# Performance work log

Measured on AMD Instinct MI355X. Metric: run time of the kernel, lower is better.

The kernel has to match this reference:

```python
import jax, jax.numpy as jnp
import numpy as np

B, T, LEADS = 16, 3600, 12
P = 9; S = T // P          # 400 patches
DP = 128                   # d_patch / codebook dim
DM = 256                   # d_model
H = 8; HD = DM // H        # heads, head_dim
NL = 6                     # transformer layers
V = 512                    # codebook size
RH = 64                    # residual CNN hidden
BETA = 0.25


def conv1d(x, w, b, pad, stride=1):
    # x: (B,C,T), w: (O,I,K) pytorch layout
    y = jax.lax.conv_general_dilated(x, w, (stride,), [(pad, pad)],
                                     dimension_numbers=('NCH', 'OIH', 'NCH'))
    return y + b[None, :, None]


def layer_norm(x, g, b, eps=1e-5):
    m = jnp.mean(x, -1, keepdims=True)
    v = jnp.mean(jnp.square(x - m), -1, keepdims=True)
    return (x - m) * jax.lax.rsqrt(v + eps) * g + b


def gelu(x):
    return jax.nn.gelu(x, approximate=False)  # matches torch nn.GELU default


def setup_inputs() -> dict:
    key = jax.random.key(0)
    ks = iter(jax.random.split(key, 64))
    def rn(shape, s=0.02):
        return (s * jax.random.normal(next(ks), shape)).astype(jnp.float32)
    inp = {}
    inp['x'] = jax.random.normal(next(ks), (B, T, LEADS), dtype=jnp.float32)
    # PatchEncoder
    inp['pe_w1'] = rn((DP // 2, LEADS, 3)); inp['pe_b1'] = rn((DP // 2,))
    inp['pe_w2'] = rn((DP, DP // 2, 3));    inp['pe_b2'] = rn((DP,))
    inp['pe_pw'] = rn((DP, DP, P));         inp['pe_pb'] = rn((DP,))
    inp['pe_g'] = jnp.ones((DP,), jnp.float32); inp['pe_bb'] = jnp.zeros((DP,), jnp.float32)
    # VQ codebook (uniform +-1/V as in torch init)
    inp['cb'] = jax.random.uniform(next(ks), (V, DP), jnp.float32, -1.0 / V, 1.0 / V)
    # token_proj
    inp['tp_w'] = rn((DM, DP)); inp['tp_b'] = rn((DM,))
    inp['tp_g'] = jnp.ones((DM,), jnp.float32); inp['tp_bb'] = jnp.zeros((DM,), jnp.float32)
    # transformer layers (stacked over NL)
    inp['ln1_g'] = jnp.ones((NL, DM), jnp.float32); inp['ln1_b'] = jnp.zeros((NL, DM), jnp.float32)
    inp['inw'] = rn((NL, 3 * DM, DM));  inp['inb'] = rn((NL, 3 * DM))
    inp['ow'] = rn((NL, DM, DM));       inp['ob'] = rn((NL, DM))
    inp['ln2_g'] = jnp.ones((NL, DM), jnp.float32); inp['ln2_b'] = jnp.zeros((NL, DM), jnp.float32)
    inp['f1w'] = rn((NL, 4 * DM, DM));  inp['f1b'] = rn((NL, 4 * DM))
    inp['f2w'] = rn((NL, DM, 4 * DM));  inp['f2b'] = rn((NL, DM))
    inp['slopes'] = (1.0 + 0.1 * jax.random.normal(next(ks), (NL, H))).astype(jnp.float32)
    # final norm
    inp['fn_g'] = jnp.ones((DM,), jnp.float32); inp['fn_b'] = jnp.zeros((DM,), jnp.float32)
    # PatchDecoder: ConvTranspose1d weight (in=DM, out=DM//2, k=P)
    inp['up_w'] = rn((DM, DM // 2, P)); inp['up_b'] = rn((DM // 2,))
    inp['d1w'] = rn((DM // 4, DM // 2, 5)); inp['d1b'] = rn((DM // 4,))
    inp['d2w'] = rn((LEADS, DM // 4, 3));   inp['d2b'] = rn((LEADS,))
    # ResidualCNN
    inp['r1w'] = rn((RH, LEADS, 7)); inp['r1b'] = rn((RH,))
    inp['r2w'] = rn((RH, RH, 5));    inp['r2b'] = rn((RH,))
    inp['r3w'] = rn((RH, RH, 3));    inp['r3b'] = rn((RH,))
    inp['r4w'] = rn((LEADS, RH, 1)); inp['r4b'] = rn((LEADS,))
    inp['alpha'] = jnp.float32(0.5)
    return inp


def _forward(x, pe_w1, pe_b1, pe_w2, pe_b2, pe_pw, pe_pb, pe_g, pe_bb, cb,
             tp_w, tp_b, tp_g, tp_bb, ln1_g, ln1_b, inw, inb, ow, ob,
             ln2_g, ln2_b, f1w, f1b, f2w, f2b, slopes, fn_g, fn_b,
             up_w, up_b, d1w, d1b, d2w, d2b,
             r1w, r1b, r2w, r2b, r3w, r3b, r4w, r4b, alpha):
    Bs = x.shape[0]
    sg = jax.lax.stop_gradient
    # --- PatchEncoder: (B,T,L) -> (B,S,DP) ---
    h = x.transpose(0, 2, 1)                      # (B,L,T)
    h = gelu(conv1d(h, pe_w1, pe_b1, 1))
    h = gelu(conv1d(h, pe_w2, pe_b2, 1))
    h = conv1d(h, pe_pw, pe_pb, 0, stride=P)      # (B,DP,S)
    z_e = layer_norm(h.transpose(0, 2, 1), pe_g, pe_bb)   # (B,S,DP)
    # --- VQ codebook with STE ---
    zf = z_e.reshape(-1, DP)
    dist = (jnp.sum(zf * zf, 1, keepdims=True) + jnp.sum(cb * cb, 1)[None, :]
            - 2.0 * zf @ cb.T)                    # (B*S, V)
    tokens = jnp.argmin(dist, axis=1)
    zq = cb[tokens]                               # (B*S, DP)
    commit = jnp.mean(jnp.square(sg(zq) - zf)) + BETA * jnp.mean(jnp.square(zq - sg(zf)))
    zq_ste = (zf + sg(zq - zf)).reshape(Bs, S, DP)
    # --- token projection ---
    h = layer_norm(zq_ste @ tp_w.T + tp_b, tp_g, tp_bb)   # (B,S,DM)
    # --- transformer with relative-position bias ---
    pos = jnp.arange(S)
    rel = jnp.abs(pos[:, None] - pos[None, :]).astype(h.dtype)  # (S,S)
    scale = 1.0 / jnp.sqrt(jnp.float32(HD))
    for l in range(NL):
        bias = -jnp.abs(slopes[l])[:, None, None] * rel[None]   # (H,S,S)
        xn = layer_norm(h, ln1_g[l], ln1_b[l])
        qkv = xn @ inw[l].T + inb[l]
        q, k, v = jnp.split(qkv, 3, axis=-1)
        q = q.reshape(Bs, S, H, HD); k = k.reshape(Bs, S, H, HD); v = v.reshape(Bs, S, H, HD)
        logits = jnp.einsum('bqhd,bkhd->bhqk', q, k) * scale + bias[None]
        attn = jax.nn.softmax(logits, axis=-1)
        o = jnp.einsum('bhqk,bkhd->bqhd', attn, v).reshape(Bs, S, DM)
        h = h + o @ ow[l].T + ob[l]
        hn = layer_norm(h, ln2_g[l], ln2_b[l])
        h = h + gelu(hn @ f1w[l].T + f1b[l]) @ f2w[l].T + f2b[l]
    h = layer_norm(h, fn_g, fn_b)
    # --- PatchDecoder: (B,S,DM) -> (B,T,L) ---
    hc = h.transpose(0, 2, 1)                     # (B,DM,S)
    # ConvTranspose1d with stride==kernel==P, no overlap -> pure einsum
    u = jnp.einsum('bds,dok->bosk', hc, up_w).reshape(Bs, DM // 2, S * P) + up_b[None, :, None]
    u = gelu(u)
    u = gelu(conv1d(u, d1w, d1b, 2))
    u = conv1d(u, d2w, d2b, 1)                    # (B,L,T)
    decoded = u.transpose(0, 2, 1)
    # --- ResidualCNN on raw input ---
    r = x.transpose(0, 2, 1)
    r = gelu(conv1d(r, r1w, r1b, 3))
    r = gelu(conv1d(r, r2w, r2b, 2))
    r = gelu(conv1d(r, r3w, r3b, 1))
    r = conv1d(r, r4w, r4b, 0)
    residual = r.transpose(0, 2, 1)
    out = decoded + alpha * residual
    return out, commit


def reference(x, pe_w1, pe_b1, pe_w2, pe_b2, pe_pw, pe_pb, pe_g, pe_bb, cb,
              tp_w, tp_b, tp_g, tp_bb, ln1_g, ln1_b, inw, inb, ow, ob,
              ln2_g, ln2_b, f1w, f1b, f2w, f2b, slopes, fn_g, fn_b,
              up_w, up_b, d1w, d1b, d2w, d2b,
              r1w, r1b, r2w, r2b, r3w, r3b, r4w, r4b, alpha):
    return _forward(x, pe_w1, pe_b1, pe_w2, pe_b2, pe_pw, pe_pb, pe_g, pe_bb, cb,
                    tp_w, tp_b, tp_g, tp_bb, ln1_g, ln1_b, inw, inb, ow, ob,
                    ln2_g, ln2_b, f1w, f1b, f2w, f2b, slopes, fn_g, fn_b,
                    up_w, up_b, d1w, d1b, d2w, d2b,
                    r1w, r1b, r2w, r2b, r3w, r3b, r4w, r4b, alpha)
```

## Files before the change

### kernel.cpp

```cpp
#include <hip/hip_runtime.h>
#include <hip/hip_bf16.h>
#include <math.h>

#define BATCH 16
#define TLEN 3600
#define LEADS 12
#define PP 9
#define SS 400
#define DP 128
#define DM 256
#define NH 8
#define HD 32
#define NLAY 6
#define VV 512
#define RH 64

typedef __attribute__((ext_vector_type(8))) short short8b;
typedef __attribute__((ext_vector_type(4))) float f32x4;

__device__ __forceinline__ float gelu_f(float x) {
    return 0.5f * x * (1.0f + erff(x * 0.70710678118654752f));
}

__device__ __forceinline__ unsigned short f2bf(float f) {
// ... 352 lines not shown
                #pragma unroll
                for (int e = 0; e < 8; ++e) {
                    unsigned short h = f2bf(vv[e]);
                    h8[e] = (short)h;
                    l8[e] = (short)f2bf(vv[e] - bf2f(h));
                }
                *(short8b*)&Ah[srow][sc + g * 8] = h8;
                *(short8b*)&Al[srow][sc + g * 8] = l8;
            }
            const unsigned short* gh = ch + (size_t)(c0 + srow) * DP + k0 + sc;
            const unsigned short* gl = cl + (size_t)(c0 + srow) * DP + k0 + sc;
            *(short8b*)&Bh[srow][sc] = *(const short8b*)gh;
            *(short8b*)&Bh[srow][sc + 8] = *(const short8b*)(gh + 8);
            *(short8b*)&Bl[srow][sc] = *(const short8b*)gl;
            *(short8b*)&Bl[srow][sc + 8] = *(const short8b*)(gl + 8);
        }
        __syncthreads();
        short8b afh[4], afl[4], bfh[4], bfl[4];
        #pragma unroll
        for (int i = 0; i < 4; ++i) {
            afh[i] = *(const short8b*)&Ah[wr0 + i * 16 + fr][kg];
            afl[i] = *(const short8b*)&Al[wr0 + i * 16 + fr][kg];
            bfh[i] = *(const short8b*)&Bh[wc0 + i * 16 + fr][kg];
            bfl[i] = *(const short8b*)&Bl[wc0 + i * 16 + fr][kg];
        }
        #pragma unroll
        for (int i = 0; i < 4; ++i)
            #pragma unroll
            for (int j = 0; j < 4; ++j) {
                acc[i][j] = __builtin_amdgcn_mfma_f32_16x16x32_bf16(afh[i], bfh[j], acc[i][j], 0, 0, 0);
                acc[i][j] = __builtin_amdgcn_mfma_f32_16x16x32_bf16(afh[i], bfl[j], acc[i][j], 0, 0, 0);
                acc[i][j] = __builtin_amdgcn_mfma_f32_16x16x32_bf16(afl[i], bfh[j], acc[i][j], 0, 0, 0);
            }
    }
    const int orow = (lane >> 4) * 4, ocol = lane & 15;
    #pragma unroll
    for (int i = 0; i < 4; ++i)
        #pragma unroll
        for (int r = 0; r < 4; ++r) {
            int row = wr0 + i * 16 + orow + r;
            float bv = 1e30f; int bi = 0;
            #pragma unroll
            for (int j = 0; j < 4; ++j) {
                int col = c0 + wc0 + j * 16 + ocol;
                float d = cbn[col] - 2.0f * acc[i][j][r];
                if (d < bv || (d == bv && col < bi)) { bv = d; bi = col; }
            }
            #pragma unroll
            for (int o = 1; o < 16; o <<= 1) {
                float ov = __shfl_xor(bv, o);
                int oi = __shfl_xor(bi, o);
                if (ov < bv || (ov == bv && oi < bi)) { bv = ov; bi = oi; }
            }
            if (ocol == 0) { bwv[row][w & 1] = bv; bwi[row][w & 1] = bi; }
        }
    __syncthreads();
    if (tid < 128) {
        float v0 = bwv[tid][0], v1 = bwv[tid][1];
        int i0 = bwi[tid][0], i1 = bwi[tid][1];
        bool sel = (v1 < v0) || (v1 == v0 && i1 < i0);
        pval[(size_t)blockIdx.x * M + gm0 + tid] = sel ? v1 : v0;
        pidx[(size_t)blockIdx.x * M + gm0 + tid] = sel ? i1 : i0;
    }
}

__global__ __launch_bounds__(128) void vqfin_k(const float* __restrict__ ze,
                                               const float* __restrict__ cb,
                                               const float* __restrict__ pval,
                                               const int* __restrict__ pidx,
                                               unsigned short* __restrict__ zqb,
                                               float* __restrict__ vqs,
                                               int M) {
    const int row = blockIdx.x, tid = threadIdx.x;
    __shared__ float sm[2];
    __shared__ int tok_s;
    if (tid == 0) {
        float bv = pval[row]; int bi = pidx[row];
        #pragma unroll
        for (int z = 1; z < 4; ++z) {
            float v = pval[(size_t)z * M + row]; int ix = pidx[(size_t)z * M + row];
            if (v < bv || (v == bv && ix < bi)) { bv = v; bi = ix; }
        }
        tok_s = bi;
    }
    __syncthreads();
    int tok = tok_s;
    float qv = cb[(size_t)tok * DP + tid];
    float zv = ze[(size_t)row * DP + tid];
    zqb[(size_t)row * DP + tid] = f2bf(qv);
    float d = qv - zv;
    float tot = block_sum_128(d * d, sm);
    if (tid == 0) vqs[row] = tot;
}

template <int CI, int K, int PAD>
__global__ __launch_bounds__(256) void mfconv_k(const unsigned short* __restrict__ in,
                                                const unsigned short* __restrict__ wpk,
                                                const float* __restrict__ bias,
                                                unsigned short* __restrict__ out) {
    constexpr int CIC = (CI > 64) ? 64 : CI;
    constexpr int NCH = CI / CIC;
    constexpr int TROWS = 128 + K - 1;
    constexpr int CQ = CIC / 8;
    __shared__ __align__(16) unsigned short in_s[TROWS][CIC + 8];
    __shared__ __align__(16) unsigned short w_s[K][64][CIC + 8];
    const int b = blockIdx.z;
    const int t0 = blockIdx.x * 128;
    const int tid = threadIdx.x;
    const int w = tid >> 6, lane = tid & 63;
    const int fr = lane & 15, kg = (lane >> 4) * 8;
    f32x4 acc[2][4];
    #pragma unroll
    for (int i = 0; i < 2; ++i)
        #pragma unroll
        for (int j = 0; j < 4; ++j) acc[i][j] = (f32x4){0.f, 0.f, 0.f, 0.f};
    for (int ch = 0; ch < NCH; ++ch) {
        const int c0 = ch * CIC;
        if (ch) __syncthreads();
        for (int u = tid; u < TROWS * CQ; u += 256) {
            int row = u / CQ, q = u - row * CQ;
            int t = t0 + row - PAD;
            short8b v = (short8b){0, 0, 0, 0, 0, 0, 0, 0};
            if (t >= 0 && t < TLEN)
                v = *(const short8b*)&in[((size_t)(b * TLEN + t)) * CI + c0 + q * 8];
            *(short8b*)&in_s[row][q * 8] = v;
        }
        for (int u = tid; u < K * 64 * CQ; u += 256) {
            int q = u % CQ; int rest = u / CQ; int co = rest & 63; int k = rest >> 6;
            *(short8b*)&w_s[k][co][q * 8] =
                *(const short8b*)&wpk[((size_t)(k * 64 + co)) * CI + c0 + q * 8];
        }
        __syncthreads();
        #pragma unroll
        for (int k = 0; k < K; ++k) {
            #pragma unroll
            for (int c32 = 0; c32 < CIC / 32; ++c32) {
                short8b a0 = *(const short8b*)&in_s[w * 32 + fr + k][c32 * 32 + kg];
                short8b a1 = *(const short8b*)&in_s[w * 32 + 16 + fr + k][c32 * 32 + kg];
                short8b b0 = *(const short8b*)&w_s[k][fr][c32 * 32 + kg];
                short8b b1 = *(const short8b*)&w_s[k][16 + fr][c32 * 32 + kg];
                short8b b2 = *(const short8b*)&w_s[k][32 + fr][c32 * 32 + kg];
                short8b b3 = *(const short8b*)&w_s[k][48 + fr][c32 * 32 + kg];
                acc[0][0] = __builtin_amdgcn_mfma_f32_16x16x32_bf16(a0, b0, acc[0][0], 0, 0, 0);
                acc[0][1] = __builtin_amdgcn_mfma_f32_16x16x32_bf16(a0, b1, acc[0][1], 0, 0, 0);
                acc[0][2] = __builtin_amdgcn_mfma_f32_16x16x32_bf16(a0, b2, acc[0][2], 0, 0, 0);
                acc[0][3] = __builtin_amdgcn_mfma_f32_16x16x32_bf16(a0, b3, acc[0][3], 0, 0, 0);
                acc[1][0] = __builtin_amdgcn_mfma_f32_16x16x32_bf16(a1, b0, acc[1][0], 0, 0, 0);
                acc[1][1] = __builtin_amdgcn_mfma_f32_16x16x32_bf16(a1, b1, acc[1][1], 0, 0, 0);
                acc[1][2] = __builtin_amdgcn_mfma_f32_16x16x32_bf16(a1, b2, acc[1][2], 0, 0, 0);
                acc[1][3] = __builtin_amdgcn_mfma_f32_16x16x32_bf16(a1, b3, acc[1][3], 0, 0, 0);
            }
        }
    }
    const int orow = (lane >> 4) * 4, ocol = lane & 15;
    #pragma unroll
    for (int i = 0; i < 2; ++i)
        #pragma unroll
        for (int j = 0; j < 4; ++j) {
            const int co = j * 16 + ocol;
            const float bv = bias[co];
            #pragma unroll
            for (int r = 0; r < 4; ++r) {
                int t = t0 + w * 32 + i * 16 + orow + r;
                if (t < TLEN)
                    out[((size_t)(b * TLEN + t)) * 64 + co] = f2bf(gelu_f(acc[i][j][r] + bv));
            }
        }
}

template <int ACT, int RES, int OUTBF>
__global__ __launch_bounds__(256) void bgemm_k(const unsigned short* __restrict__ A,
                                               const unsigned short* __restrict__ W,
                                               const float* __restrict__ bias,
                                               const float* __restrict__ res,
                                               void* __restrict__ Cv,
                                               int M, int N, int K) {
    __shared__ __align__(16) unsigned short As[128][40];
    __shared__ __align__(16) unsigned short Bs[128][40];
    const int tid = threadIdx.x;
    const int gm0 = blockIdx.y * 128, gn0 = blockIdx.x * 128;
    const int w = tid >> 6, lane = tid & 63;
    const int wr0 = (w >> 1) * 64, wc0 = (w & 1) * 64;
    const int srow = tid >> 1, sc = (tid & 1) * 16;
    const unsigned short* ga = A + (size_t)(gm0 + srow) * K + sc;
    const unsigned short* gb = W + (size_t)(gn0 + srow) * K + sc;
    short8b ra0 = *(const short8b*)(ga), ra1 = *(const short8b*)(ga + 8);
    short8b rb0 = *(const short8b*)(gb), rb1 = *(const short8b*)(gb + 8);
    f32x4 acc[4][4];
    #pragma unroll
    for (int i = 0; i < 4; ++i)
        #pragma unroll
        for (int j = 0; j < 4; ++j) acc[i][j] = (f32x4){0.f, 0.f, 0.f, 0.f};
    const int fr = lane & 15, kg = (lane >> 4) * 8;
    const int nstep = K >> 5;
    for (int s = 0; s < nstep; ++s) {
        __syncthreads();
        *(short8b*)&As[srow][sc] = ra0; *(short8b*)&As[srow][sc + 8] = ra1;
        *(short8b*)&Bs[srow][sc] = rb0; *(short8b*)&Bs[srow][sc + 8] = rb1;
        __syncthreads();
        if (s + 1 < nstep) {
            ga += 32; gb += 32;
            ra0 = *(const short8b*)(ga); ra1 = *(const short8b*)(ga + 8);
            rb0 = *(const short8b*)(gb); rb1 = *(const short8b*)(gb + 8);
        }
        short8b af[4], bf[4];
        #pragma unroll
        for (int i = 0; i < 4; ++i) {
            af[i] = *(const short8b*)&As[wr0 + i * 16 + fr][kg];
            bf[i] = *(const short8b*)&Bs[wc0 + i * 16 + fr][kg];
        }
        #pragma unroll
        for (int i = 0; i < 4; ++i)
            #pragma unroll
            for (int j = 0; j < 4; ++j)
                acc[i][j] = __builtin_amdgcn_mfma_f32_16x16x32_bf16(af[i], bf[j], acc[i][j], 0, 0, 0);
    }
    const int orow = (lane >> 4) * 4, ocol = lane & 15;
    #pragma unroll
    for (int i = 0; i < 4; ++i) {
        #pragma unroll
        for (int j = 0; j < 4; ++j) {
            const int colg = gn0 + wc0 + j * 16 + ocol;
            const float bsv = bias[colg];
            #pragma unroll
            for (int r = 0; r < 4; ++r) {
                const int rowg = gm0 + wr0 + i * 16 + orow + r;
                float v = acc[i][j][r] + bsv;
                if (ACT) v = gelu_f(v);
                if (RES) v += res[(size_t)rowg * N + colg];
                if (OUTBF) ((unsigned short*)Cv)[(size_t)rowg * N + colg] = f2bf(v);
                else ((float*)Cv)[(size_t)rowg * N + colg] = v;
            }
        }
    }
}

template <int ACT, int RES, int OUTBF>
__global__ __launch_bounds__(256) void bgemm64_k(const unsigned short* __restrict__ A,
                                                 const unsigned short* __restrict__ W,
                                                 const float* __restrict__ bias,
                                                 const float* __restrict__ res,
                                                 void* __restrict__ Cv,
                                                 int M, int N, int K) {
    __shared__ __align__(16) unsigned short As[64][40];
    __shared__ __align__(16) unsigned short Bs[128][40];
    const int tid = threadIdx.x;
    const int gm0 = blockIdx.y * 64, gn0 = blockIdx.x * 128;
    const int w = tid >> 6, lane = tid & 63;
    const int wc0 = w * 32;
    const int arow = tid >> 2, ac = (tid & 3) * 8;
    const int brow = tid >> 1, bc = (tid & 1) * 16;
    const unsigned short* ga = A + (size_t)(gm0 + arow) * K + ac;
    const unsigned short* gb = W + (size_t)(gn0 + brow) * K + bc;
    short8b ra0 = *(const short8b*)(ga);
    short8b rb0 = *(const short8b*)(gb), rb1 = *(const short8b*)(gb + 8);
    f32x4 acc[4][2];
    #pragma unroll
    for (int i = 0; i < 4; ++i)
        #pragma unroll
        for (int j = 0; j < 2; ++j) acc[i][j] = (f32x4){0.f, 0.f, 0.f, 0.f};
    const int fr = lane & 15, kg = (lane >> 4) * 8;
    const int nstep = K >> 5;
    for (int s = 0; s < nstep; ++s) {
        __syncthreads();
        *(short8b*)&As[arow][ac] = ra0;
        *(short8b*)&Bs[brow][bc] = rb0; *(short8b*)&Bs[brow][bc + 8] = rb1;
        __syncthreads();
        if (s + 1 < nstep) {
            ga += 32; gb += 32;
            ra0 = *(const short8b*)(ga);
            rb0 = *(const short8b*)(gb); rb1 = *(const short8b*)(gb + 8);
        }
        short8b af[4], bf[2];
        #pragma unroll
        for (int i = 0; i < 4; ++i) af[i] = *(const short8b*)&As[i * 16 + fr][kg];
        #pragma unroll
        for (int j = 0; j < 2; ++j) bf[j] = *(const short8b*)&Bs[wc0 + j * 16 + fr][kg];
        #pragma unroll
        for (int i = 0; i < 4; ++i)
            #pragma unroll
            for (int j = 0; j < 2; ++j)
                acc[i][j] = __builtin_amdgcn_mfma_f32_16x16x32_bf16(af[i], bf[j], acc[i][j], 0, 0, 0);
    }
    const int orow = (lane >> 4) * 4, ocol = lane & 15;
    #pragma unroll
    for (int i = 0; i < 4; ++i) {
        #pragma unroll
        for (int j = 0; j < 2; ++j) {
            const int colg = gn0 + wc0 + j * 16 + ocol;
            const float bsv = bias[colg];
            #pragma unroll
            for (int r = 0; r < 4; ++r) {
                const int rowg = gm0 + i * 16 + orow + r;
                float v = acc[i][j][r] + bsv;
                if (ACT) v = gelu_f(v);
                if (RES) v += res[(size_t)rowg * N + colg];
                if (OUTBF) ((unsigned short*)Cv)[(size_t)rowg * N + colg] = f2bf(v);
                else ((float*)Cv)[(size_t)rowg * N + colg] = v;
            }
        }
    }
}

__global__ void tobf_k(const float* __restrict__ in, unsigned short* __restrict__ out, int n) {
    int i = blockIdx.x * 256 + threadIdx.x;
    if (i < n) out[i] = f2bf(in[i]);
}

__global__ void cpack_k(const float* __restrict__ w, unsigned short* __restrict__ out,
                        int Co, int CI, int K) {
    int idx = blockIdx.x * 256 + threadIdx.x;
    if (idx < Co * CI * K) {
        int ci = idx % CI; int rest = idx / CI; int co = rest % Co; int k = rest / Co;
        out[idx] = f2bf(w[((size_t)co * CI + ci) * K + k]);
    }
}

__global__ void upwt2_k(const float* __restrict__ w, const float* __restrict__ bsrc,
                        unsigned short* __restrict__ out, float* __restrict__ b2) {
    int idx = blockIdx.x * 256 + threadIdx.x;
    if (idx < 1152 * 256) {
        int d = idx & 255, n = idx >> 8;
        int o = n & 127, k = n >> 7;
        out[(size_t)n * 256 + d] = f2bf(w[(size_t)d * 1152 + o * 9 + k]);
    }
    if (idx < 1152) b2[idx] = bsrc[idx & 127];
}

__global__ __launch_bounds__(128) void ln128s_k(const float* __restrict__ part,
                                                const float* __restrict__ bias,
                                                const float* __restrict__ g,
                                                const float* __restrict__ bb,
                                                float* __restrict__ out,
                                                int M) {
    int row = blockIdx.x, tid = threadIdx.x;
    __shared__ float sm[2];
    size_t stride = (size_t)M * DP;
    size_t base = (size_t)row * DP + tid;
    float v = bias[tid];
    #pragma unroll
    for (int s2 = 0; s2 < 6; ++s2) v += part[base + (size_t)s2 * stride];
    float mean = block_sum_128(v, sm) * (1.0f / DP);
    float d = v - mean;
    float var = block_sum_128(d * d, sm) * (1.0f / DP);
    out[(size_t)row * DP + tid] = d * rsqrtf(var + 1e-5f) * g[tid] + bb[tid];
}

__global__ void cbnorm_k(const float* __restrict__ cb, float* __restrict__ cbn) {
    int c = blockIdx.x * 256 + threadIdx.x;
    if (c < VV) {
        const float* cr = cb + (size_t)c * DP;
        float s = 0;
        for (int i = 0; i < DP; ++i) s += cr[i] * cr[i];
        cbn[c] = s;
    }
}

__global__ void vqreduce_k(const float* __restrict__ vqs, float* __restrict__ out) {
    float s = 0;
    for (int i = threadIdx.x; i < BATCH * SS; i += 256) s += vqs[i];
    __shared__ float sm[4];
    s = block_sum_256(s, sm);
    if (threadIdx.x == 0) out[0] = s * (1.25f / (float)(BATCH * SS * DP));
}

template <int OUTBF>
__global__ __launch_bounds__(256) void lnw_k(const float* __restrict__ in,
                                             const float* __restrict__ g,
                                             const float* __restrict__ bb,
                                             void* __restrict__ out) {
    const int row = blockIdx.x * 4 + (threadIdx.x >> 6);
    const int lane = threadIdx.x & 63;
    float4 v = *(const float4*)&in[(size_t)row * DM + lane * 4];
    float s = v.x + v.y + v.z + v.w;
    #pragma unroll
    for (int o = 1; o < 64; o <<= 1) s += __shfl_xor(s, o);
    float mean = s * (1.0f / DM);
    float dx = v.x - mean, dy = v.y - mean, dz = v.z - mean, dw = v.w - mean;
    float vv = dx * dx + dy * dy + dz * dz + dw * dw;
    #pragma unroll
    for (int o = 1; o < 64; o <<= 1) vv += __shfl_xor(vv, o);
    float rstd = rsqrtf(vv * (1.0f / DM) + 1e-5f);
    float4 gv = *(const float4*)&g[lane * 4];
    float4 bv = *(const float4*)&bb[lane * 4];
    float o0 = dx * rstd * gv.x + bv.x;
    float o1 = dy * rstd * gv.y + bv.y;
    float o2 = dz * rstd * gv.z + bv.z;
    float o3 = dw * rstd * gv.w + bv.w;
    if (OUTBF) {
        unsigned long long pk = (unsigned long long)f2bf(o0)
                              | ((unsigned long long)f2bf(o1) << 16)
                              | ((unsigned long long)f2bf(o2) << 32)
                              | ((unsigned long long)f2bf(o3) << 48);
        *(unsigned long long*)((unsigned short*)out + (size_t)row * DM + lane * 4) = pk;
    } else {
        float4 o4; o4.x = o0; o4.y = o1; o4.z = o2; o4.w = o3;
        *(float4*)((float*)out + (size_t)row * DM + lane * 4) = o4;
    }
}

__global__ __launch_bounds__(256) void fattn2_k(const unsigned short* __restrict__ qkv,
                                                const float* __restrict__ slopes,
                                                unsigned short* __restrict__ out) {
    __shared__ __align__(16) unsigned short Qs[128][40];
    __shared__ __align__(16) unsigned short Ks[64][40];
    __shared__ __align__(16) unsigned short Vt[32][72];
    __shared__ __align__(16) unsigned short Ps[4][32][72];
    const int qb = blockIdx.x, hh = blockIdx.y, b = blockIdx.z;
    const int tid = threadIdx.x;
    const int w = tid >> 6, lane = tid & 63;
    const int lr = lane & 15, lg = lane >> 4;
    const float slope = fabsf(slopes[hh]);
    const unsigned short* base = qkv + (size_t)b * SS * (3 * DM);
    {
        int row = tid >> 1, c = (tid & 1) * 16;
        int q = qb * 128 + row; q = q < SS ? q : SS - 1;
        const unsigned short* src = base + (size_t)q * (3 * DM) + hh * HD + c;
        *(short8b*)&Qs[row][c] = *(const short8b*)src;
        *(short8b*)&Qs[row][c + 8] = *(const short8b*)(src + 8);
    }
    __syncthreads();
    short8b qa[2];
    qa[0] = *(const short8b*)&Qs[w * 32 + lr][lg * 8];
    qa[1] = *(const short8b*)&Qs[w * 32 + 16 + lr][lg * 8];
    float m_run[2][4], l_run[2][4];
    #pragma unroll
    for (int f = 0; f < 2; ++f)
        #pragma unroll
        for (int r = 0; r < 4; ++r) { m_run[f][r] = -1e30f; l_run[f][r] = 0.f; }
    f32x4 of0[2], of1[2];
    of0[0] = of0[1] = of1[0] = of1[1] = (f32x4){0.f, 0.f, 0.f, 0.f};
    const int qg0[2] = { qb * 128 + w * 32 + lg * 4, qb * 128 + w * 32 + 16 + lg * 4 };
    for (int kt = 0; kt < SS; kt += 64) {
        const int tl = (SS - kt) < 64 ? (SS - kt) : 64;
        const int nks = tl >> 4;
        __syncthreads();
        {
            int row = tid >> 2, c = (tid & 3) * 8;
            if (row < tl) {
                *(short8b*)&Ks[row][c] =
                    *(const short8b*)(base + (size_t)(kt + row) * (3 * DM) + DM + hh * HD + c);
                short8b v8 = *(const short8b*)(base + (size_t)(kt + row) * (3 * DM) + 2 * DM + hh * HD + c);
                #pragma unroll
                for (int j = 0; j < 8; ++j) Vt[c + j][row] = ((unsigned short*)&v8)[j];
            }
        }
        __syncthreads();
        f32x4 sf[2][4];
        #pragma unroll
        for (int ks = 0; ks < 4; ++ks) {
            if (ks < nks) {
                short8b kb8 = *(const short8b*)&Ks[ks * 16 + lr][lg * 8];
                sf[0][ks] = __builtin_amdgcn_mfma_f32_16x16x32_bf16(qa[0], kb8, (f32x4){0.f, 0.f, 0.f, 0.f}, 0, 0, 0);
                sf[1][ks] = __builtin_amdgcn_mfma_f32_16x16x32_bf16(qa[1], kb8, (f32x4){0.f, 0.f, 0.f, 0.f}, 0, 0, 0);
            }
        }
        #pragma unroll
        for (int f = 0; f < 2; ++f) {
            float pv[4][4];
            #pragma unroll
            for (int r = 0; r < 4; ++r) {
                float tmax = -1e30f;
                #pragma unroll
                for (int ks = 0; ks < 4; ++ks) {
                    if (ks < nks) {
                        float sv = sf[f][ks][r] * 0.17677669529663687f
                                 - slope * fabsf((float)(qg0[f] + r - (kt + ks * 16 + lr)));
                        pv[ks][r] = sv;
                        tmax = fmaxf(tmax, sv);
                    }
                }
                #pragma unroll
                for (int o = 1; o < 16; o <<= 1) tmax = fmaxf(tmax, __shfl_xor(tmax, o));
                float mnew = fmaxf(m_run[f][r], tmax);
                float sc = __expf(m_run[f][r] - mnew);
                m_run[f][r] = mnew;
                float tsum = 0.f;
                #pragma unroll
                for (int ks = 0; ks < 4; ++ks) {
                    if (ks < nks) {
                        float e = __expf(pv[ks][r] - mnew);
                        pv[ks][r] = e;
                        tsum += e;
                    }
                }
                #pragma unroll
                for (int o = 1; o < 16; o <<= 1) tsum += __shfl_xor(tsum, o);
                l_run[f][r] = l_run[f][r] * sc + tsum;
                of0[f][r] *= sc; of1[f][r] *= sc;
            }
            #pragma unroll
            for (int ks = 0; ks < 4; ++ks)
                #pragma unroll
                for (int r = 0; r < 4; ++r)
                    Ps[w][f * 16 + lg * 4 + r][ks * 16 + lr] = (ks < nks) ? f2bf(pv[ks][r]) : (unsigned short)0;
        }
        #pragma unroll
        for (int kc = 0; kc < 64; kc += 32) {
            if (kc < nks * 16) {
                short8b vb0 = *(const short8b*)&Vt[lr][kc + lg * 8];
                short8b vb1 = *(const short8b*)&Vt[16 + lr][kc + lg * 8];
                #pragma unroll
                for (int f = 0; f < 2; ++f) {
                    short8b pa = *(const short8b*)&Ps[w][f * 16 + lr][kc + lg * 8];
                    of0[f] = __builtin_amdgcn_mfma_f32_16x16x32_bf16(pa, vb0, of0[f], 0, 0, 0);
                    of1[f] = __builtin_amdgcn_mfma_f32_16x16x32_bf16(pa, vb1, of1[f], 0, 0, 0);
                }
            }
        }
    }
    #pragma unroll
    for (int f = 0; f < 2; ++f)
        #pragma unroll
        for (int r = 0; r < 4; ++r) {
            int q = qg0[f] + r;
            if (q < SS) {
                float inv = 1.0f / l_run[f][r];
                out[((size_t)(b * SS + q)) * DM + hh * HD + lr] = f2bf(of0[f][r] * inv);
                out[((size_t)(b * SS + q)) * DM + hh * HD + 16 + lr] = f2bf(of1[f][r] * inv);
            }
        }
}

__global__ __launch_bounds__(256) void final2_k(const unsigned short* __restrict__ ud1,
                                                const unsigned short* __restrict__ r3i,
                                                const float* __restrict__ d2w,
                                                const float* __restrict__ d2b,
                                                const float* __restrict__ r4w,
                                                const float* __restrict__ r4b,
                                                const float* __restrict__ alpha,
                                                float* __restrict__ out) {
    __shared__ float u_s[64][66];
    __shared__ float r_s[64][64];
    __shared__ float wd_s[64][3][12];
    __shared__ float wr_s[64][12];
    __shared__ float o_s[64][12];
    const int b = blockIdx.z, t0 = blockIdx.x * 64, tid = threadIdx.x;
    for (int u2 = tid; u2 < 66 * 8; u2 += 256) {
        int j = u2 >> 3, q = u2 & 7;
        int t = t0 + j - 1;
        short8b v = (short8b){0, 0, 0, 0, 0, 0, 0, 0};
        if (t >= 0 && t < TLEN) v = *(const short8b*)&ud1[((size_t)(b * TLEN + t)) * 64 + q * 8];
        #pragma unroll
        for (int i = 0; i < 8; ++i) u_s[q * 8 + i][j] = bf2f((unsigned short)v[i]);
    }
    for (int u2 = tid; u2 < 64 * 8; u2 += 256) {
        int j = u2 >> 3, q = u2 & 7;
        int t = t0 + j;
        short8b v = (short8b){0, 0, 0, 0, 0, 0, 0, 0};
        if (t < TLEN) v = *(const short8b*)&r3i[((size_t)(b * TLEN + t)) * 64 + q * 8];
        #pragma unroll
        for (int i = 0; i < 8; ++i) r_s[q * 8 + i][j] = bf2f((unsigned short)v[i]);
    }
    for (int idx = tid; idx < 64 * 3 * 12; idx += 256) {
        int l = idx % 12, k = (idx / 12) % 3, ci = idx / 36;
        wd_s[ci][k][l] = d2w[(l * 64 + ci) * 3 + k];
    }
    for (int idx = tid; idx < 64 * 12; idx += 256) {
        int l = idx % 12, ci = idx / 12;
        wr_s[ci][l] = r4w[l * 64 + ci];
    }
    __syncthreads();
    const int tl = tid & 63, lg = tid >> 6;
    float accD[3] = {}, accR[3] = {};
    for (int ci = 0; ci < 64; ++ci) {
        float a0 = u_s[ci][tl], a1 = u_s[ci][tl + 1], a2 = u_s[ci][tl + 2];
        float rv = r_s[ci][tl];
        #pragma unroll
        for (int c = 0; c < 3; ++c) {
            int l = lg * 3 + c;
            accD[c] += a0 * wd_s[ci][0][l] + a1 * wd_s[ci][1][l] + a2 * wd_s[ci][2][l];
            accR[c] = fmaf(rv, wr_s[ci][l], accR[c]);
        }
    }
    float al = alpha[0];
    #pragma unroll
    for (int c = 0; c < 3; ++c) {
        int l = lg * 3 + c;
        o_s[tl][l] = accD[c] + d2b[l] + al * (accR[c] + r4b[l]);
    }
    __syncthreads();
    for (int idx = tid; idx < 64 * 12; idx += 256) {
        int t = t0 + idx / 12;
        if (t < TLEN) out[((size_t)b * TLEN + t) * 12 + idx % 12] = o_s[idx / 12][idx % 12];
    }
}

extern "C" void kernel_launch(void* const* d_in, const int* in_sizes, int n_in,
                              void* d_out, int out_size, void* d_ws, size_t ws_size,
                              hipStream_t stream) {
    const float* x     = (const float*)d_in[0];
    const float* pe_w1 = (const float*)d_in[1];
    const float* pe_b1 = (const float*)d_in[2];
    const float* pe_w2 = (const float*)d_in[3];
    const float* pe_b2 = (const float*)d_in[4];
    const float* pe_pw = (const float*)d_in[5];
    const float* pe_pb = (const float*)d_in[6];
    const float* pe_g  = (const float*)d_in[7];
    const float* pe_bb = (const float*)d_in[8];
    const float* cb    = (const float*)d_in[9];
    const float* tp_w  = (const float*)d_in[10];
    const float* tp_b  = (const float*)d_in[11];
    const float* tp_g  = (const float*)d_in[12];
    const float* tp_bb = (const float*)d_in[13];
    const float* ln1_g = (const float*)d_in[14];
    const float* ln1_b = (const float*)d_in[15];
    const float* inw   = (const float*)d_in[16];
    const float* inb   = (const float*)d_in[17];
    const float* ow    = (const float*)d_in[18];
    const float* ob    = (const float*)d_in[19];
    const float* ln2_g = (const float*)d_in[20];
    const float* ln2_b = (const float*)d_in[21];
    const float* f1w   = (const float*)d_in[22];
    const float* f1b   = (const float*)d_in[23];
    const float* f2w   = (const float*)d_in[24];
    const float* f2b   = (const float*)d_in[25];
    const float* slopes= (const float*)d_in[26];
    const float* fn_g  = (const float*)d_in[27];
    const float* fn_b  = (const float*)d_in[28];
    const float* up_w  = (const float*)d_in[29];
    const float* up_b  = (const float*)d_in[30];
    const float* d1w   = (const float*)d_in[31];
    const float* d1b   = (const float*)d_in[32];
    const float* d2w   = (const float*)d_in[33];
    const float* d2b   = (const float*)d_in[34];
    const float* r1w   = (const float*)d_in[35];
    const float* r1b   = (const float*)d_in[36];
    const float* r2w   = (const float*)d_in[37];
    const float* r2b   = (const float*)d_in[38];
    const float* r3w   = (const float*)d_in[39];
    const float* r3b   = (const float*)d_in[40];
    const float* r4w   = (const float*)d_in[41];
    const float* r4b   = (const float*)d_in[42];
    const float* alpha = (const float*)d_in[43];

    float* W = (float*)d_ws;
    size_t off = 0;
    auto alloc = [&](size_t n) { float* p = W + off; off += (n + 3) & ~(size_t)3; return p; };
    const size_t M = (size_t)BATCH * SS;
    float* A    = alloc((size_t)BATCH * DP * TLEN);
    float* Bb   = alloc((size_t)BATCH * 64 * TLEN);
    float* ze   = alloc(M * DP);
    float* tx   = alloc(M * DM);
    float* hb   = alloc(M * DM);
    float* qf   = alloc(M * 3 * DM);
    float* cbn  = alloc(VV);
    float* vqs  = alloc(M);
    float* upb2 = alloc(1152);
    float* pval = alloc(4 * M);
    int*   pidx = (int*)alloc(4 * M);
    unsigned short* zqb  = (unsigned short*)alloc(M * DP / 2);
    unsigned short* xnb  = (unsigned short*)alloc(M * DM / 2);
    unsigned short* aob  = (unsigned short*)alloc(M * DM / 2);
    float* pgpart        = qf;
    unsigned short* qkvb = (unsigned short*)qf;
    unsigned short* ffb  = (unsigned short*)qf;
    unsigned short* utm  = (unsigned short*)qf;
    unsigned short* inwb = (unsigned short*)alloc((size_t)NLAY * 3 * DM * DM / 2);
    unsigned short* owb  = (unsigned short*)alloc((size_t)NLAY * DM * DM / 2);
    unsigned short* f1wb = (unsigned short*)alloc((size_t)NLAY * 4 * DM * DM / 2);
    unsigned short* f2wb = (unsigned short*)alloc((size_t)NLAY * 4 * DM * DM / 2);
    unsigned short* tpwb = (unsigned short*)alloc((size_t)DM * DP / 2);
    unsigned short* upwb = (unsigned short*)alloc((size_t)1152 * DM / 2);
    unsigned short* pwh  = (unsigned short*)alloc((size_t)128 * 1152 / 2);
    unsigned short* pwl  = (unsigned short*)alloc((size_t)128 * 1152 / 2);
    unsigned short* w2h  = (unsigned short*)alloc((size_t)3 * 128 * 64 / 2);
    unsigned short* w2l  = (unsigned short*)alloc((size_t)3 * 128 * 64 / 2);
    unsigned short* cbh  = (unsigned short*)alloc((size_t)VV * DP / 2);
    unsigned short* cbl  = (unsigned short*)alloc((size_t)VV * DP / 2);
    unsigned short* r2pk = (unsigned short*)alloc((size_t)64 * 64 * 5 / 2);
    unsigned short* r3pk = (unsigned short*)alloc((size_t)64 * 64 * 3 / 2 + 2);
    unsigned short* d1pk = (unsigned short*)alloc((size_t)64 * 128 * 5 / 2);
    unsigned short* r1tm = (unsigned short*)alloc((size_t)BATCH * TLEN * 64 / 2);
    unsigned short* r2tm = (unsigned short*)alloc((size_t)BATCH * TLEN * 64 / 2);
    unsigned short* r3tm = (unsigned short*)alloc((size_t)BATCH * TLEN * 64 / 2);
    unsigned short* d1tm = (unsigned short*)alloc((size_t)BATCH * TLEN * 64 / 2);
    if (off * sizeof(float) > ws_size) return;

    float* outp = (float*)d_out;
    const dim3 cgrid(57, 1, BATCH);
    const dim3 mgrid(29, 1, BATCH);

    tobf_k<<<(NLAY * 3 * DM * DM + 255) / 256, 256, 0, stream>>>(inw, inwb, NLAY * 3 * DM * DM);
    tobf_k<<<(NLAY * DM * DM + 255) / 256, 256, 0, stream>>>(ow, owb, NLAY * DM * DM);
    tobf_k<<<(NLAY * 4 * DM * DM + 255) / 256, 256, 0, stream>>>(f1w, f1wb, NLAY * 4 * DM * DM);
    tobf_k<<<(NLAY * 4 * DM * DM + 255) / 256, 256, 0, stream>>>(f2w, f2wb, NLAY * 4 * DM * DM);
    tobf_k<<<(DM * DP + 255) / 256, 256, 0, stream>>>(tp_w, tpwb, DM * DP);
    upwt2_k<<<(1152 * 256 + 255) / 256, 256, 0, stream>>>(up_w, up_b, upwb, upb2);
    pwpack3_k<<<(128 * 1152 + 255) / 256, 256, 0, stream>>>(pe_pw, pwh, pwl);
    pwpack2_k<<<(3 * 128 * 64 + 255) / 256, 256, 0, stream>>>(pe_w2, w2h, w2l);
    cbpack_k<<<(VV * DP + 255) / 256, 256, 0, stream>>>(cb, cbh, cbl);
    cpack_k<<<(64 * 64 * 5 + 255) / 256, 256, 0, stream>>>(r2w, r2pk, 64, 64, 5);
    cpack_k<<<(64 * 64 * 3 + 255) / 256, 256, 0, stream>>>(r3w, r3pk, 64, 64, 3);
    cpack_k<<<(64 * 128 * 5 + 255) / 256, 256, 0, stream>>>(d1w, d1pk, 64, 128, 5);

    enc1_k<<<dim3(57, BATCH), 256, 0, stream>>>(x, pe_w1, pe_b1, r1w, r1b, Bb, r1tm);

    pe2m_k<<<dim3(29, BATCH), 256, 0, stream>>>(Bb, w2h, w2l, pe_b2, A);
    cbnorm_k<<<2, 256, 0, stream>>>(cb, cbn);
    pproj3_k<<<dim3(1, M / 128, 6), 256, 0, stream>>>(A, pwh, pwl, pgpart, M);
    ln128s_k<<<M, 128, 0, stream>>>(pgpart, pe_pb, pe_g, pe_bb, ze, M);
    vq3_k<<<dim3(4, M / 128), 256, 0, stream>>>(ze, cbh, cbl, cbn, pval, pidx, M);
    vqfin_k<<<M, 128, 0, stream>>>(ze, cb, pval, pidx, zqb, vqs, M);
    vqreduce_k<<<1, 256, 0, stream>>>(vqs, outp + (size_t)BATCH * TLEN * LEADS);

    mfconv_k<64, 5, 2><<<mgrid, 256, 0, stream>>>(r1tm, r2pk, r2b, r2tm);
    mfconv_k<64, 3, 1><<<mgrid, 256, 0, stream>>>(r2tm, r3pk, r3b, r3tm);

    bgemm64_k<0, 0, 0><<<dim3(DM / 128, M / 64), 256, 0, stream>>>(zqb, tpwb, tp_b, nullptr, tx, M, DM, DP);
    lnw_k<0><<<M / 4, 256, 0, stream>>>(tx, tp_g, tp_bb, hb);

    for (int l = 0; l < NLAY; ++l) {
        lnw_k<1><<<M / 4, 256, 0, stream>>>(hb, ln1_g + l * DM, ln1_b + l * DM, xnb);
        bgemm_k<0, 0, 1><<<dim3(3 * DM / 128, M / 128), 256, 0, stream>>>(
            xnb, inwb + (size_t)l * 3 * DM * DM, inb + l * 3 * DM, nullptr, qkvb, M, 3 * DM, DM);
        fattn2_k<<<dim3((SS + 127) / 128, NH, BATCH), 256, 0, stream>>>(qkvb, slopes + l * NH, aob);
        bgemm64_k<0, 1, 0><<<dim3(DM / 128, M / 64), 256, 0, stream>>>(
            aob, owb + (size_t)l * DM * DM, ob + l * DM, hb, hb, M, DM, DM);
        lnw_k<1><<<M / 4, 256, 0, stream>>>(hb, ln2_g + l * DM, ln2_b + l * DM, xnb);
        bgemm_k<1, 0, 1><<<dim3(4 * DM / 128, M / 128), 256, 0, stream>>>(
            xnb, f1wb + (size_t)l * 4 * DM * DM, f1b + l * 4 * DM, nullptr, ffb, M, 4 * DM, DM);
        bgemm64_k<0, 1, 0><<<dim3(DM / 128, M / 64), 256, 0, stream>>>(
            ffb, f2wb + (size_t)l * 4 * DM * DM, f2b + l * DM, hb, hb, M, DM, 4 * DM);
    }
    lnw_k<1><<<M / 4, 256, 0, stream>>>(hb, fn_g, fn_b, xnb);

    bgemm_k<1, 0, 1><<<dim3(1152 / 128, M / 128), 256, 0, stream>>>(xnb, upwb, upb2, nullptr, utm, M, 1152, DM);
    mfconv_k<128, 5, 2><<<mgrid, 256, 0, stream>>>(utm, d1pk, d1b, d1tm);

    final2_k<<<cgrid, 256, 0, stream>>>(d1tm, r3tm, d2w, d2b, r4w, r4b, alpha, outp);
}
```

Measured before the change: 790.2 us.

## Fuse residual GEMMs with following LayerNorm and shrink attention query tile

Adds a GEMM kernel that computes a full 256-wide output row block (32 rows per block), adds bias and residual, writes the fp32 hidden state, then applies the next LayerNorm in-kernel and writes the bf16 normalized input. This replaces the separate out-proj/FFN2 GEMMs and the LN launches inside the layer loop, removing launches and a reread of the hidden state. Attention is changed to 64-query tiles (one 16-row fragment per wave), doubling the grid for better occupancy at the cost of reloading K/V more often. The fused GEMM uses a small 32-row tile and unpipelined register prefetch, which may lower MFMA efficiency.

```diff
diff --git a/kernel.cpp b/kernel.cpp
--- a/kernel.cpp
+++ b/kernel.cpp
@@ -678,6 +678,99 @@
     }
 }
 
+__global__ __launch_bounds__(256) void bgemmln_k(const unsigned short* __restrict__ A,
+                                                 const unsigned short* __restrict__ W,
+                                                 const float* __restrict__ bias,
+                                                 const float* __restrict__ res,
+                                                 float* __restrict__ hbout,
+                                                 const float* __restrict__ g,
+                                                 const float* __restrict__ bb,
+                                                 unsigned short* __restrict__ xout,
+                                                 int M, int K) {
+    __shared__ __align__(16) char smem[33792];
+    unsigned short (*As)[40] = (unsigned short(*)[40])smem;
+    unsigned short (*Bs)[40] = (unsigned short(*)[40])(smem + 2560);
+    float (*Ct)[264] = (float(*)[264])smem;
+    const int tid = threadIdx.x;
+    const int gm0 = blockIdx.x * 32;
+    const int w = tid >> 6, lane = tid & 63;
+    const int wc0 = w * 64;
+    const int fr = lane & 15, kg = (lane >> 4) * 8;
+    const unsigned short* ga = A + (size_t)(gm0 + (tid >> 2)) * K + (tid & 3) * 8;
+    const unsigned short* gb = W + (size_t)tid * K;
+    short8b ra;
+    if (tid < 128) ra = *(const short8b*)ga;
+    short8b rb0 = *(const short8b*)(gb), rb1 = *(const short8b*)(gb + 8);
+    short8b rb2 = *(const short8b*)(gb + 16), rb3 = *(const short8b*)(gb + 24);
+    f32x4 acc[2][4];
+    #pragma unroll
+    for (int i = 0; i < 2; ++i)
+        #pragma unroll
+        for (int j = 0; j < 4; ++j) acc[i][j] = (f32x4){0.f, 0.f, 0.f, 0.f};
+    const int nstep = K >> 5;
+    for (int s = 0; s < nstep; ++s) {
+        __syncthreads();
+        if (tid < 128) *(short8b*)&As[tid >> 2][(tid & 3) * 8] = ra;
+        *(short8b*)&Bs[tid][0] = rb0;  *(short8b*)&Bs[tid][8] = rb1;
+        *(short8b*)&Bs[tid][16] = rb2; *(short8b*)&Bs[tid][24] = rb3;
+        __syncthreads();
+        if (s + 1 < nstep) {
+            ga += 32; gb += 32;
+            if (tid < 128) ra = *(const short8b*)ga;
+            rb0 = *(const short8b*)(gb);      rb1 = *(const short8b*)(gb + 8);
+            rb2 = *(const short8b*)(gb + 16); rb3 = *(const short8b*)(gb + 24);
+        }
+        short8b af[2], bf[4];
+        af[0] = *(const short8b*)&As[fr][kg];
+        af[1] = *(const short8b*)&As[16 + fr][kg];
+        #pragma unroll
+        for (int j = 0; j < 4; ++j) bf[j] = *(const short8b*)&Bs[wc0 + j * 16 + fr][kg];
+        #pragma unroll
+        for (int i = 0; i < 2; ++i)
+            #pragma unroll
+            for (int j = 0; j < 4; ++j)
+                acc[i][j] = __builtin_amdgcn_mfma_f32_16x16x32_bf16(af[i], bf[j], acc[i][j], 0, 0, 0);
+    }
+    __syncthreads();
+    const int orow = (lane >> 4) * 4, ocol = lane & 15;
+    #pragma unroll
+    for (int i = 0; i < 2; ++i)
+        #pragma unroll
+        for (int j = 0; j < 4; ++j) {
+            const int col = wc0 + j * 16 + ocol;
+            const float bsv = bias[col];
+            #pragma unroll
+            for (int r = 0; r < 4; ++r) {
+                const int row = i * 16 + orow + r;
+                float v = acc[i][j][r] + bsv + res[(size_t)(gm0 + row) * DM + col];
+                hbout[(size_t)(gm0 + row) * DM + col] = v;
+                Ct[row][col] = v;
+            }
+        }
+    __syncthreads();
+    #pragma unroll
+    for (int rr = 0; rr < 8; ++rr) {
+        const int row = w * 8 + rr;
+        float4 v = *(const float4*)&Ct[row][lane * 4];
+        float s = v.x + v.y + v.z + v.w;
+        #pragma unroll
+        for (int o = 1; o < 64; o <<= 1) s += __shfl_xor(s, o);
+        float mean = s * (1.0f / DM);
+        float dx = v.x - mean, dy = v.y - mean, dz = v.z - mean, dw = v.w - mean;
+        float vv = dx * dx + dy * dy + dz * dz + dw * dw;
+        #pragma unroll
+        for (int o = 1; o < 64; o <<= 1) vv += __shfl_xor(vv, o);
+        float rstd = rsqrtf(vv * (1.0f / DM) + 1e-5f);
+        float4 gv = *(const float4*)&g[lane * 4];
+        float4 bv = *(const float4*)&bb[lane * 4];
+        unsigned long long pk = (unsigned long long)f2bf(dx * rstd * gv.x + bv.x)
+                              | ((unsigned long long)f2bf(dy * rstd * gv.y + bv.y) << 16)
+                              | ((unsigned long long)f2bf(dz * rstd * gv.z + bv.z) << 32)
+                              | ((unsigned long long)f2bf(dw * rstd * gv.w + bv.w) << 48);
+        *(unsigned long long*)&xout[(size_t)(gm0 + row) * DM + lane * 4] = pk;
+    }
+}
+
 __global__ void tobf_k(const float* __restrict__ in, unsigned short* __restrict__ out, int n) {
     int i = blockIdx.x * 256 + threadIdx.x;
     if (i < n) out[i] = f2bf(in[i]);
@@ -775,13 +868,13 @@
     }
 }
 
-__global__ __launch_bounds__(256) void fattn2_k(const unsigned short* __restrict__ qkv,
-                                                const float* __restrict__ slopes,
-                                                unsigned short* __restrict__ out) {
-    __shared__ __align__(16) unsigned short Qs[128][40];
+__global__ __launch_bounds__(256) void fattn_k(const unsigned short* __restrict__ qkv,
+                                               const float* __restrict__ slopes,
+                                               unsigned short* __restrict__ out) {
+    __shared__ __align__(16) unsigned short Qs[64][40];
     __shared__ __align__(16) unsigned short Ks[64][40];
     __shared__ __align__(16) unsigned short Vt[32][72];
-    __shared__ __align__(16) unsigned short Ps[4][32][72];
+    __shared__ __align__(16) unsigned short Ps[4][16][72];
     const int qb = blockIdx.x, hh = blockIdx.y, b = blockIdx.z;
     const int tid = threadIdx.x;
     const int w = tid >> 6, lane = tid & 63;
@@ -789,24 +882,16 @@
     const float slope = fabsf(slopes[hh]);
     const unsigned short* base = qkv + (size_t)b * SS * (3 * DM);
     {
-        int row = tid >> 1, c = (tid & 1) * 16;
-        int q = qb * 128 + row; q = q < SS ? q : SS - 1;
-        const unsigned short* src = base + (size_t)q * (3 * DM) + hh * HD + c;
-        *(short8b*)&Qs[row][c] = *(const short8b*)src;
-        *(short8b*)&Qs[row][c + 8] = *(const short8b*)(src + 8);
+        int row = tid >> 2, c = (tid & 3) * 8;
+        int q = qb * 64 + row; q = q < SS ? q : SS - 1;
+        *(short8b*)&Qs[row][c] = *(const short8b*)(base + (size_t)q * (3 * DM) + hh * HD + c);
     }
     __syncthreads();
-    short8b qa[2];
-    qa[0] = *(const short8b*)&Qs[w * 32 + lr][lg * 8];
-    qa[1] = *(const short8b*)&Qs[w * 32 + 16 + lr][lg * 8];
-    float m_run[2][4], l_run[2][4];
-    #pragma unroll
-    for (int f = 0; f < 2; ++f)
-        #pragma unroll
-        for (int r = 0; r < 4; ++r) { m_run[f][r] = -1e30f; l_run[f][r] = 0.f; }
-    f32x4 of0[2], of1[2];
-    of0[0] = of0[1] = of1[0] = of1[1] = (f32x4){0.f, 0.f, 0.f, 0.f};
-    const int qg0[2] = { qb * 128 + w * 32 + lg * 4, qb * 128 + w * 32 + 16 + lg * 4 };
+    const short8b qa = *(const short8b*)&Qs[w * 16 + lr][lg * 8];
+    float m_run[4] = {-1e30f, -1e30f, -1e30f, -1e30f};
+    float l_run[4] = {0.f, 0.f, 0.f, 0.f};
+    f32x4 of0 = (f32x4){0.f, 0.f, 0.f, 0.f}, of1 = (f32x4){0.f, 0.f, 0.f, 0.f};
+    const int qg0 = qb * 64 + w * 16 + lg * 4;
     for (int kt = 0; kt < SS; kt += 64) {
         const int tl = (SS - kt) < 64 ? (SS - kt) : 64;
         const int nks = tl >> 4;
@@ -822,80 +907,71 @@
             }
         }
         __syncthreads();
-        f32x4 sf[2][4];
+        f32x4 sf[4];
         #pragma unroll
         for (int ks = 0; ks < 4; ++ks) {
             if (ks < nks) {
-                short8b kb8 = *(const short8b*)&Ks[ks * 16 + lr][lg * 8];
-                sf[0][ks] = __builtin_amdgcn_mfma_f32_16x16x32_bf16(qa[0], kb8, (f32x4){0.f, 0.f, 0.f, 0.f}, 0, 0, 0);
-                sf[1][ks] = __builtin_amdgcn_mfma_f32_16x16x32_bf16(qa[1], kb8, (f32x4){0.f, 0.f, 0.f, 0.f}, 0, 0, 0);
-            }
-        }
-        #pragma unroll
-        for (int f = 0; f < 2; ++f) {
-            float pv[4][4];
-            #pragma unroll
-            for (int r = 0; r < 4; ++r) {
-                float tmax = -1e30f;
-                #pragma unroll
-                for (int ks = 0; ks < 4; ++ks) {
-                    if (ks < nks) {
-                        float sv = sf[f][ks][r] * 0.17677669529663687f
-                                 - slope * fabsf((float)(qg0[f] + r - (kt + ks * 16 + lr)));
-                        pv[ks][r] = sv;
-                        tmax = fmaxf(tmax, sv);
-                    }
+                short8b kb = *(const short8b*)&Ks[ks * 16 + lr][lg * 8];
+                sf[ks] = __builtin_amdgcn_mfma_f32_16x16x32_bf16(qa, kb, (f32x4){0.f, 0.f, 0.f, 0.f}, 0, 0, 0);
+            }
+        }
+        float pv[4][4];
+        #pragma unroll
+        for (int r = 0; r < 4; ++r) {
+            float tmax = -1e30f;
+            #pragma unroll
+            for (int ks = 0; ks < 4; ++ks) {
+                if (ks < nks) {
+                    float sv = sf[ks][r] * 0.17677669529663687f
+                             - slope * fabsf((float)(qg0 + r - (kt + ks * 16 + lr)));
+                    pv[ks][r] = sv;
+                    tmax = fmaxf(tmax, sv);
                 }
-                #pragma unroll
-                for (int o = 1; o < 16; o <<= 1) tmax = fmaxf(tmax, __shfl_xor(tmax, o));
-                float mnew = fmaxf(m_run[f][r], tmax);
-                float sc = __expf(m_run[f][r] - mnew);
-                m_run[f][r] = mnew;
-                float tsum = 0.f;
-                #pragma unroll
-                for (int ks = 0; ks < 4; ++ks) {
-                    if (ks < nks) {
-                        float e = __expf(pv[ks][r] - mnew);
-                        pv[ks][r] = e;
-                        tsum += e;
-                    }
+            }
+            #pragma unroll
+            for (int o = 1; o < 16; o <<= 1) tmax = fmaxf(tmax, __shfl_xor(tmax, o));
+            float mnew = fmaxf(m_run[r], tmax);
+            float sc = __expf(m_run[r] - mnew);
+            m_run[r] = mnew;
+            float tsum = 0.f;
+            #pragma unroll
+            for (int ks = 0; ks < 4; ++ks) {
+                if (ks < nks) {
+                    float e = __expf(pv[ks][r] - mnew);
+                    pv[ks][r] = e;
+                    tsum += e;
                 }
-                #pragma unroll
-                for (int o = 1; o < 16; o <<= 1) tsum += __shfl_xor(tsum, o);
-                l_run[f][r] = l_run[f][r] * sc + tsum;
-                of0[f][r] *= sc; of1[f][r] *= sc;
-            }
-            #pragma unroll
-            for (int ks = 0; ks < 4; ++ks)
-                #pragma unroll
-                for (int r = 0; r < 4; ++r)
-                    Ps[w][f * 16 + lg * 4 + r][ks * 16 + lr] = (ks < nks) ? f2bf(pv[ks][r]) : (unsigned short)0;
-        }
+            }
+            #pragma unroll
+            for (int o = 1; o < 16; o <<= 1) tsum += __shfl_xor(tsum, o);
+            l_run[r] = l_run[r] * sc + tsum;
+            of0[r] *= sc; of1[r] *= sc;
+        }
+        #pragma unroll
+        for (int ks = 0; ks < 4; ++ks)
+            #pragma unroll
+            for (int r = 0; r < 4; ++r)
+                Ps[w][lg * 4 + r][ks * 16 + lr] = (ks < nks) ? f2bf(pv[ks][r]) : (unsigned short)0;
         #pragma unroll
         for (int kc = 0; kc < 64; kc += 32) {
             if (kc < nks * 16) {
+                short8b pa = *(const short8b*)&Ps[w][lr][kc + lg * 8];
                 short8b vb0 = *(const short8b*)&Vt[lr][kc + lg * 8];
                 short8b vb1 = *(const short8b*)&Vt[16 + lr][kc + lg * 8];
-                #pragma unroll
-                for (int f = 0; f < 2; ++f) {
-                    short8b pa = *(const short8b*)&Ps[w][f * 16 + lr][kc + lg * 8];
-                    of0[f] = __builtin_amdgcn_mfma_f32_16x16x32_bf16(pa, vb0, of0[f], 0, 0, 0);
-                    of1[f] = __builtin_amdgcn_mfma_f32_16x16x32_bf16(pa, vb1, of1[f], 0, 0, 0);
-                }
-            }
-        }
-    }
-    #pragma unroll
-    for (int f = 0; f < 2; ++f)
-        #pragma unroll
-        for (int r = 0; r < 4; ++r) {
-            int q = qg0[f] + r;
-            if (q < SS) {
-                float inv = 1.0f / l_run[f][r];
-                out[((size_t)(b * SS + q)) * DM + hh * HD + lr] = f2bf(of0[f][r] * inv);
-                out[((size_t)(b * SS + q)) * DM + hh * HD + 16 + lr] = f2bf(of1[f][r] * inv);
-            }
-        }
+                of0 = __builtin_amdgcn_mfma_f32_16x16x32_bf16(pa, vb0, of0, 0, 0, 0);
+                of1 = __builtin_amdgcn_mfma_f32_16x16x32_bf16(pa, vb1, of1, 0, 0, 0);
+            }
+        }
+    }
+    #pragma unroll
+    for (int r = 0; r < 4; ++r) {
+        int q = qg0 + r;
+        if (q < SS) {
+            float inv = 1.0f / l_run[r];
+            out[((size_t)(b * SS + q)) * DM + hh * HD + lr] = f2bf(of0[r] * inv);
+            out[((size_t)(b * SS + q)) * DM + hh * HD + 16 + lr] = f2bf(of1[r] * inv);
+        }
+    }
 }
 
 __global__ __launch_bounds__(256) void final2_k(const unsigned short* __restrict__ ud1,
@@ -1085,21 +1161,23 @@
 
     bgemm64_k<0, 0, 0><<<dim3(DM / 128, M / 64), 256, 0, stream>>>(zqb, tpwb, tp_b, nullptr, tx, M, DM, DP);
     lnw_k<0><<<M / 4, 256, 0, stream>>>(tx, tp_g, tp_bb, hb);
+    lnw_k<1><<<M / 4, 256, 0, stream>>>(hb, ln1_g, ln1_b, xnb);
 
     for (int l = 0; l < NLAY; ++l) {
-        lnw_k<1><<<M / 4, 256, 0, stream>>>(hb, ln1_g + l * DM, ln1_b + l * DM, xnb);
         bgemm_k<0, 0, 1><<<dim3(3 * DM / 128, M / 128), 256, 0, stream>>>(
             xnb, inwb + (size_t)l * 3 * DM * DM, inb + l * 3 * DM, nullptr, qkvb, M, 3 * DM, DM);
-        fattn2_k<<<dim3((SS + 127) / 128, NH, BATCH), 256, 0, stream>>>(qkvb, slopes + l * NH, aob);
-        bgemm64_k<0, 1, 0><<<dim3(DM / 128, M / 64), 256, 0, stream>>>(
-            aob, owb + (size_t)l * DM * DM, ob + l * DM, hb, hb, M, DM, DM);
-        lnw_k<1><<<M / 4, 256, 0, stream>>>(hb, ln2_g + l * DM, ln2_b + l * DM, xnb);
+        fattn_k<<<dim3((SS + 63) / 64, NH, BATCH), 256, 0, stream>>>(qkvb, slopes + l * NH, aob);
+        bgemmln_k<<<M / 32, 256, 0, stream>>>(
+            aob, owb + (size_t)l * DM * DM, ob + l * DM, hb, hb,
+            ln2_g + l * DM, ln2_b + l * DM, xnb, M, DM);
         bgemm_k<1, 0, 1><<<dim3(4 * DM / 128, M / 128), 256, 0, stream>>>(
             xnb, f1wb + (size_t)l * 4 * DM * DM, f1b + l * 4 * DM, nullptr, ffb, M, 4 * DM, DM);
-        bgemm64_k<0, 1, 0><<<dim3(DM / 128, M / 64), 256, 0, stream>>>(
-            ffb, f2wb + (size_t)l * 4 * DM * DM, f2b + l * DM, hb, hb, M, DM, 4 * DM);
-    }
-    lnw_k<1><<<M / 4, 256, 0, stream>>>(hb, fn_g, fn_b, xnb);
+        const float* gN = (l < NLAY - 1) ? ln1_g + (l + 1) * DM : fn_g;
+        const float* bN = (l < NLAY - 1) ? ln1_b + (l + 1) * DM : fn_b;
+        bgemmln_k<<<M / 32, 256, 0, stream>>>(
+            ffb, f2wb + (size_t)l * 4 * DM * DM, f2b + l * DM, hb, hb,
+            gN, bN, xnb, M, 4 * DM);
+    }
 
     bgemm_k<1, 0, 1><<<dim3(1152 / 128, M / 128), 256, 0, stream>>>(xnb, upwb, upb2, nullptr, utm, M, 1152, DM);
     mfconv_k<128, 5, 2><<<mgrid, 256, 0, stream>>>(utm, d1pk, d1b, d1tm);
```

New measurement: 818.3 us. 1.04x slower.
